# Performance work log

Hardware: AMD Instinct MI355X
Metric: run time of the kernel (lower is better)

## Reference

```python
import jax, jax.numpy as jnp
import numpy as np

N = 100000      # nodes
E = 1_600_000   # edges (avg degree 16)
IN, HID, OUT = 128, 128, 64


def _prep(edge_index, n):
    """Add self-loops and compute symmetric GCN normalization per edge."""
    loops = jnp.arange(n, dtype=edge_index.dtype)
    src = jnp.concatenate([edge_index[0], loops])  # [E+N]
    dst = jnp.concatenate([edge_index[1], loops])  # [E+N]
    deg = jax.ops.segment_sum(jnp.ones(src.shape, jnp.float32), dst, num_segments=n)
    dinv = jnp.where(deg > 0, jax.lax.rsqrt(deg), 0.0)
    norm = dinv[src] * dinv[dst]                   # [E+N]
    return src, dst, norm


def gcn_conv(x, src, dst, norm, W, b, n):
    # PyG GCNConv: transform first, then normalized gather/scatter-add aggregate
    h = x @ W                                      # [N, C_out]
    msg = h[src] * norm[:, None]                   # [E+N, C_out] irregular gather
    return jax.ops.segment_sum(msg, dst, num_segments=n) + b


def setup_inputs() -> dict:
    key = jax.random.key(0)
    k1, k2, k3, k4 = jax.random.split(key, 4)
    x = jax.random.normal(k1, (N, IN), dtype=jnp.float32)
    edge_index = jax.random.randint(k2, (2, E), 0, N, dtype=jnp.int32)
    W1 = jax.random.normal(k3, (IN, HID), dtype=jnp.float32) * (1.0 / np.sqrt(IN))
    b1 = jnp.zeros((HID,), jnp.float32)
    W2 = jax.random.normal(k4, (HID, OUT), dtype=jnp.float32) * (1.0 / np.sqrt(HID))
    b2 = jnp.zeros((OUT,), jnp.float32)
    return {"x": x, "W1": W1, "b1": b1, "W2": W2, "b2": b2, "edge_index": edge_index}


def reference(x, W1, b1, W2, b2, edge_index):
    n = x.shape[0]
    src, dst, norm = _prep(edge_index, n)
    h = gcn_conv(x, src, dst, norm, W1, b1, n)
    h = jax.nn.softmax(h, axis=1)
    return gcn_conv(h, src, dst, norm, W2, b2, n)
```

## Files before the change

### kernel.cpp

```cpp
#include <hip/hip_runtime.h>
#include <hip/hip_fp16.h>
#include <cstdint>
#include <cstddef>


#define BSHIFT 8
#define NBPAD 512
#define NWG 256
#define CAP 6144

typedef _Float16 half8 __attribute__((ext_vector_type(8)));
typedef float f32x4 __attribute__((ext_vector_type(4)));

__device__ __forceinline__ void h8_to_f(const uint4& u, float* f) {
  const __half2* hp = (const __half2*)&u;
#pragma unroll
  for (int i = 0; i < 4; ++i) {
    float2 t = __half22float2(hp[i]);
    f[2 * i] = t.x;
    f[2 * i + 1] = t.y;
  }
}

__device__ __forceinline__ void fma8(float* acc, float w, const float* v) {
#pragma unroll
  for (int i = 0; i < 8; ++i) acc[i] = fmaf(w, v[i], acc[i]);
}

__device__ __forceinline__ int block_scan256(int v, int* wsums) {
  const int lane = threadIdx.x & 63;
  const int wid = threadIdx.x >> 6;
  int x = v;
#pragma unroll
  for (int d = 1; d < 64; d <<= 1) {
    int y = __shfl_up(x, d);
    if (lane >= d) x += y;
  }
  if (lane == 63) wsums[wid] = x;
  __syncthreads();
  int off = 0;
#pragma unroll
  for (int j = 0; j < 4; ++j)
    if (j < wid) off += wsums[j];
  return off + x;
}

__global__ __launch_bounds__(256) void wg_count(const int* __restrict__ dst,
                                                int* __restrict__ counts,
                                                int E, int nb, int slice) {
  __shared__ int lh[NBPAD];
  const int w = blockIdx.x;
  for (int i = threadIdx.x; i < nb; i += 256) lh[i] = 0;
  __syncthreads();
  const int e0 = w * slice;
  const int e1 = min(e0 + slice, E);
  for (int e = e0 + threadIdx.x; e < e1; e += 256)
    atomicAdd(&lh[dst[e] >> BSHIFT], 1);
  __syncthreads();
  for (int i = threadIdx.x; i < nb; i += 256) counts[(size_t)w * NBPAD + i] = lh[i];
}

__global__ __launch_bounds__(256) void cell_scan(const int* __restrict__ counts,
                                                 int* __restrict__ cur,
                                                 int* __restrict__ btotal, int nb) {
  __shared__ int wsums[4];
  const int b = blockIdx.x;
  const int tid = threadIdx.x;
  int v = counts[(size_t)tid * NBPAD + b];
  int incl = block_scan256(v, wsums);
  cur[(size_t)tid * NBPAD + b] = incl - v;
  if (tid == 255) btotal[b] = incl;
}

__global__ __launch_bounds__(1024) void bscan(const int* __restrict__ btotal,
                                              int* __restrict__ bstart,
                                              int* __restrict__ row_start,
                                              int nb, int n, int E) {
  __shared__ int wsum[16];
  const int tid = threadIdx.x;
  const int lane = tid & 63;
  const int wid = tid >> 6;
  int v = (tid < nb) ? btotal[tid] : 0;
  int x = v;
#pragma unroll
  for (int d = 1; d < 64; d <<= 1) {
    int y = __shfl_up(x, d);
    if (lane >= d) x += y;
  }
  if (lane == 63) wsum[wid] = x;
  __syncthreads();
  if (wid == 0) {
    int w = (lane < 16) ? wsum[lane] : 0;
#pragma unroll
    for (int d = 1; d < 16; d <<= 1) {
      int y = __shfl_up(w, d);
      if (lane >= d) w += y;
    }
    if (lane < 16) wsum[lane] = w;
  }
  __syncthreads();
  int boff = (wid > 0) ? wsum[wid - 1] : 0;
  int incl = boff + x;
  if (tid < nb) {
    bstart[tid] = incl - v;
    if (tid == nb - 1) bstart[nb] = incl;
  }
  if (tid == 0) row_start[n] = E;
}

__global__ __launch_bounds__(256) void wg_scatter(const int* __restrict__ src,
                                                  const int* __restrict__ dst,
                                                  const int* __restrict__ cur,
                                                  const int* __restrict__ bstart,
                                                  unsigned* __restrict__ staging,
                                                  int E, int nb, int slice) {
  __shared__ int lc[NBPAD];
  const int w = blockIdx.x;
  for (int i = threadIdx.x; i < nb; i += 256)
    lc[i] = cur[(size_t)w * NBPAD + i] + bstart[i];
  __syncthreads();
  const int e0 = w * slice;
  const int e1 = min(e0 + slice, E);
  for (int e = e0 + threadIdx.x; e < e1; e += 256) {
    int d = dst[e];
    int p = atomicAdd(&lc[d >> BSHIFT], 1);
    staging[p] = ((unsigned)(d & 255) << 24) | (unsigned)src[e];
  }
}

__global__ __launch_bounds__(256) void bucket_hist(const unsigned* __restrict__ staging,
                                                   const int* __restrict__ bstart,
                                                   int* __restrict__ row_start,
                                                   float* __restrict__ dinv, int n) {
  __shared__ int lcnt[256];
  __shared__ int wsums[4];
  const int b = blockIdx.x;
  const int tid = threadIdx.x;
  const int n0 = b << BSHIFT;
  const int s0 = bstart[b];
  const int cnt = bstart[b + 1] - s0;

  lcnt[tid] = 0;
  __syncthreads();
  for (int i = tid; i < cnt; i += 256)
    atomicAdd(&lcnt[staging[s0 + i] >> 24], 1);
  __syncthreads();

  const int v = lcnt[tid];
  const int incl = block_scan256(v, wsums);
  const int node = n0 + tid;
  if (node < n) {
    row_start[node] = s0 + incl - v;
    dinv[node] = rsqrtf((float)v + 1.0f);
  }
}

__global__ __launch_bounds__(256) void bucket_pack(const unsigned* __restrict__ staging,
                                                   const int* __restrict__ bstart,
                                                   const int* __restrict__ row_start,
                                                   const float* __restrict__ dinv,
                                                   int2* __restrict__ pack, int n) {
  __shared__ int lcur[256];
  __shared__ int lbuf[CAP];
  const int b = blockIdx.x;
  const int tid = threadIdx.x;
  const int n0 = b << BSHIFT;
  const int s0 = bstart[b];
  const int cnt = bstart[b + 1] - s0;

  const int node = n0 + tid;
  lcur[tid] = (node < n) ? (row_start[node] - s0) : 0;
  __syncthreads();

  for (int i = tid; i < cnt; i += 256) {
    unsigned p = staging[s0 + i];
    int pos = atomicAdd(&lcur[p >> 24], 1);
    int s = (int)(p & 0xFFFFFFu);
    if (pos < CAP) lbuf[pos] = s;
    else pack[s0 + pos] = make_int2(s, __float_as_int(dinv[s]));
  }
  __syncthreads();
  const int lim = cnt < CAP ? cnt : CAP;
  for (int i = tid; i < lim; i += 256) {
    int s = lbuf[i];
    pack[s0 + i] = make_int2(s, __float_as_int(dinv[s]));
  }
}

template <int M>
__global__ __launch_bounds__(256) void pack_w(const float* __restrict__ W,
                                              _Float16* __restrict__ Wp) {
  int e = blockIdx.x * 256 + threadIdx.x;
  if (e < 128 * M) {
    int k = e / M, c = e % M;
    int t = k >> 5, g = (k >> 3) & 3, j = k & 7;
    Wp[(((size_t)t * M + c) * 4 + g) * 8 + j] = (_Float16)W[e];
  }
}

template <int M, bool HIN>
__global__ __launch_bounds__(256) void gemm_mfma(const void* __restrict__ Xp,
                                                 const _Float16* __restrict__ Wp,
                                                 _Float16* __restrict__ H, int N) {
  constexpr int CT = M / 16;
  const int wave = threadIdx.x >> 6;
  const int lane = threadIdx.x & 63;
  const int row0 = (blockIdx.x * 4 + wave) * 16;
  if (row0 >= N) return;
  const int r = lane & 15;
  const int g = lane >> 4;
  int row = row0 + r;
  if (row >= N) row = N - 1;

  f32x4 acc[CT];
#pragma unroll
  for (int c = 0; c < CT; ++c) acc[c] = (f32x4){0.f, 0.f, 0.f, 0.f};

#pragma unroll
  for (int t = 0; t < 4; ++t) {
    half8 a;
    if constexpr (HIN) {
      a = *(const half8*)((const _Float16*)Xp + (size_t)row * 128 + t * 32 + g * 8);
    } else {
      const float* xp = (const float*)Xp + (size_t)row * 128 + t * 32 + g * 8;
      float4 x0 = *(const float4*)xp;
      float4 x1 = *(const float4*)(xp + 4);
      a[0] = (_Float16)x0.x; a[1] = (_Float16)x0.y;
      a[2] = (_Float16)x0.z; a[3] = (_Float16)x0.w;
      a[4] = (_Float16)x1.x; a[5] = (_Float16)x1.y;
      a[6] = (_Float16)x1.z; a[7] = (_Float16)x1.w;
    }
#pragma unroll
    for (int c = 0; c < CT; ++c) {
      half8 b = *(const half8*)(Wp + (((size_t)t * M + c * 16 + r) * 4 + g) * 8);
      acc[c] = __builtin_amdgcn_mfma_f32_16x16x32_f16(a, b, acc[c], 0, 0, 0);
    }
  }

#pragma unroll
  for (int c = 0; c < CT; ++c) {
#pragma unroll
    for (int i = 0; i < 4; ++i) {
      int rr = row0 + 4 * g + i;
      if (rr < N) H[(size_t)rr * M + c * 16 + r] = (_Float16)acc[c][i];
    }
  }
}

__device__ __forceinline__ void pack_batch(const int2* __restrict__ pack,
                                           int e, int e1, int2* p) {
#pragma unroll
  for (int j = 0; j < 4; ++j) {
    int idx = e + j;
    bool ok = idx < e1;
    p[j] = pack[ok ? idx : (e1 - 1)];
    if (!ok) p[j].y = 0;
  }
}

template <int F, bool SM, bool OUTHALF>
__global__ __launch_bounds__(256) void aggregate(const __half* __restrict__ h,
                                                 const int* __restrict__ row_start,
                                                 const int2* __restrict__ pack,
                                                 const float* __restrict__ dinv,
                                                 const float* __restrict__ bias,
                                                 void* __restrict__ out, int n) {
  constexpr int LPG = F / 8;
  constexpr int GPB = 256 / LPG;
  const int node = blockIdx.x * GPB + (int)(threadIdx.x / LPG);
  const int lane = threadIdx.x % LPG;
  if (node >= n) return;

  const uint4* hv = (const uint4*)h;
  const float di = dinv[node];

  float acc[8];
  {
    uint4 su = hv[(size_t)node * LPG + lane];
    float sf[8];
    h8_to_f(su, sf);
#pragma unroll
    for (int i = 0; i < 8; ++i) acc[i] = di * sf[i];
  }

  const int e0 = row_start[node];
  const int e1 = row_start[node + 1];
  const int nbat = (e1 - e0 + 3) >> 2;

  if (nbat > 0) {
    int2 p0[4], p1[4];
    uint4 r0[4];
    pack_batch(pack, e0, e1, p0);
#pragma unroll
    for (int j = 0; j < 4; ++j) r0[j] = hv[(size_t)p0[j].x * LPG + lane];
    if (nbat > 1) pack_batch(pack, e0 + 4, e1, p1);

    for (int k = 0; k < nbat; ++k) {
      uint4 r1[4];
      if (k + 1 < nbat) {
#pragma unroll
        for (int j = 0; j < 4; ++j) r1[j] = hv[(size_t)p1[j].x * LPG + lane];
      }
      int2 p2[4];
      if (k + 2 < nbat) pack_batch(pack, e0 + 4 * (k + 2), e1, p2);
#pragma unroll
      for (int j = 0; j < 4; ++j) {
        float v[8];
        h8_to_f(r0[j], v);
        fma8(acc, __int_as_float(p0[j].y), v);
      }
#pragma unroll
      for (int j = 0; j < 4; ++j) {
        p0[j] = p1[j];
        p1[j] = p2[j];
        r0[j] = r1[j];
      }
    }
  }

  {
    const float4* bv = (const float4*)bias;
    float4 b0 = bv[lane * 2], b1 = bv[lane * 2 + 1];
    acc[0] = fmaf(di, acc[0], b0.x);
    acc[1] = fmaf(di, acc[1], b0.y);
    acc[2] = fmaf(di, acc[2], b0.z);
    acc[3] = fmaf(di, acc[3], b0.w);
    acc[4] = fmaf(di, acc[4], b1.x);
    acc[5] = fmaf(di, acc[5], b1.y);
    acc[6] = fmaf(di, acc[6], b1.z);
    acc[7] = fmaf(di, acc[7], b1.w);
  }

  if constexpr (SM) {
    float m = acc[0];
#pragma unroll
    for (int i = 1; i < 8; ++i) m = fmaxf(m, acc[i]);
#pragma unroll
    for (int off = LPG / 2; off >= 1; off >>= 1) m = fmaxf(m, __shfl_xor(m, off));
    float ex[8], ssum = 0.f;
#pragma unroll
    for (int i = 0; i < 8; ++i) {
      ex[i] = __expf(acc[i] - m);
      ssum += ex[i];
    }
#pragma unroll
    for (int off = LPG / 2; off >= 1; off >>= 1) ssum += __shfl_xor(ssum, off);
    float r = 1.0f / ssum;
#pragma unroll
    for (int i = 0; i < 8; ++i) acc[i] = ex[i] * r;
  }

  if constexpr (OUTHALF) {
    union { __half2 h2[4]; uint4 u; } cv;
#pragma unroll
    for (int i = 0; i < 4; ++i)
      cv.h2[i] = __floats2half2_rn(acc[2 * i], acc[2 * i + 1]);
    ((uint4*)out)[(size_t)node * LPG + lane] = cv.u;
  } else {
    float4* ov = (float4*)out;
    ov[(size_t)node * (F / 4) + lane * 2] =
        make_float4(acc[0], acc[1], acc[2], acc[3]);
    ov[(size_t)node * (F / 4) + lane * 2 + 1] =
        make_float4(acc[4], acc[5], acc[6], acc[7]);
  }
}

extern "C" void kernel_launch(void* const* d_in, const int* in_sizes, int n_in,
                              void* d_out, int out_size, void* d_ws, size_t ws_size,
                              hipStream_t stream) {
  const float* x  = (const float*)d_in[0];
  const float* W1 = (const float*)d_in[1];
  const float* b1 = (const float*)d_in[2];
  const float* W2 = (const float*)d_in[3];
  const float* b2 = (const float*)d_in[4];
  const int*   ei = (const int*)d_in[5];

  const int N = in_sizes[0] / 128;
  const int E = in_sizes[5] / 2;
  const int NB = (N + 255) >> BSHIFT;
  const int SLICE = (E + NWG - 1) / NWG;
  const int* srcp = ei;
  const int* dstp = ei + E;

  auto align256 = [](size_t v) { return (v + 255) & ~(size_t)255; };
  char* ws = (char*)d_ws;
  size_t o_dinv   = 0;
  size_t o_rs     = align256(o_dinv + (size_t)N * 4);
  size_t o_cnts   = align256(o_rs + (size_t)(N + 1) * 4);
  size_t o_cur    = align256(o_cnts + (size_t)NWG * NBPAD * 4);
  size_t o_btot   = align256(o_cur + (size_t)NWG * NBPAD * 4);
  size_t o_bstart = align256(o_btot + (size_t)NBPAD * 4);
  size_t o_wp1    = align256(o_bstart + (size_t)(NBPAD + 1) * 4);
  size_t o_wp2    = align256(o_wp1 + (size_t)128 * 128 * 2);
  size_t o_stg    = align256(o_wp2 + (size_t)128 * 64 * 2);
  size_t o_pack   = align256(o_stg + (size_t)E * 4);
  size_t o_h1     = align256(o_pack + (size_t)E * 8);
  size_t o_s      = align256(o_h1 + (size_t)N * 128 * 2);

  float*    dinv     = (float*)(ws + o_dinv);
  int*      rowstart = (int*)(ws + o_rs);
  int*      counts   = (int*)(ws + o_cnts);
  int*      cur      = (int*)(ws + o_cur);
  int*      btotal   = (int*)(ws + o_btot);
  int*      bstart   = (int*)(ws + o_bstart);
  _Float16* wp1      = (_Float16*)(ws + o_wp1);
  _Float16* wp2      = (_Float16*)(ws + o_wp2);
  unsigned* staging  = (unsigned*)(ws + o_stg);
  int2*     pack     = (int2*)(ws + o_pack);
  _Float16* h1       = (_Float16*)(ws + o_h1);
  _Float16* sbuf     = (_Float16*)(ws + o_s);

  wg_count<<<NWG, 256, 0, stream>>>(dstp, counts, E, NB, SLICE);
  cell_scan<<<NB, 256, 0, stream>>>(counts, cur, btotal, NB);
  bscan<<<1, 1024, 0, stream>>>(btotal, bstart, rowstart, NB, N, E);
  wg_scatter<<<NWG, 256, 0, stream>>>(srcp, dstp, cur, bstart, staging, E, NB, SLICE);
  bucket_hist<<<NB, 256, 0, stream>>>(staging, bstart, rowstart, dinv, N);
  bucket_pack<<<NB, 256, 0, stream>>>(staging, bstart, rowstart, dinv, pack, N);

  pack_w<128><<<(128 * 128 + 255) / 256, 256, 0, stream>>>(W1, wp1);
  pack_w<64><<<(128 * 64 + 255) / 256, 256, 0, stream>>>(W2, wp2);

  gemm_mfma<128, false><<<(N + 63) / 64, 256, 0, stream>>>(x, wp1, h1, N);
  aggregate<128, true, true><<<(N + 15) / 16, 256, 0, stream>>>(
      (const __half*)h1, rowstart, pack, dinv, b1, sbuf, N);
  gemm_mfma<64, true><<<(N + 63) / 64, 256, 0, stream>>>(sbuf, wp2, h1, N);
  aggregate<64, false, false><<<(N + 31) / 32, 256, 0, stream>>>(
      (const __half*)h1, rowstart, pack, dinv, b2, d_out, N);
}
```

Baseline: 192.4 us.

## Fold source-degree scaling into GEMM epilogue and shrink edge pack to indices

The dinv[src] factor of the symmetric normalization is now applied once per row in the GEMM epilogue, so the aggregation does plain adds instead of per-edge weighted FMAs. The per-edge pack array drops from int2 (index plus weight) to a bare int index, halving index traffic in both aggregation passes and in bucket_pack. Padded tail edges now point at an extra zero row appended to each feature buffer, which is cleared with memsets. This adds a separate h2 buffer and a per-row dinv load in the GEMMs, and multiplying before the fp16 store changes rounding slightly.

Result: no change. 195.8 us (+1.7%).

```diff
diff --git a/kernel.cpp b/kernel.cpp
--- a/kernel.cpp
+++ b/kernel.cpp
@@ -22,9 +22,9 @@
   }
 }
 
-__device__ __forceinline__ void fma8(float* acc, float w, const float* v) {
-#pragma unroll
-  for (int i = 0; i < 8; ++i) acc[i] = fmaf(w, v[i], acc[i]);
+__device__ __forceinline__ void add8(float* acc, const float* v) {
+#pragma unroll
+  for (int i = 0; i < 8; ++i) acc[i] += v[i];
 }
 
 __device__ __forceinline__ int block_scan256(int v, int* wsums) {
@@ -158,8 +158,7 @@
 __global__ __launch_bounds__(256) void bucket_pack(const unsigned* __restrict__ staging,
                                                    const int* __restrict__ bstart,
                                                    const int* __restrict__ row_start,
-                                                   const float* __restrict__ dinv,
-                                                   int2* __restrict__ pack, int n) {
+                                                   int* __restrict__ pack, int n) {
   __shared__ int lcur[256];
   __shared__ int lbuf[CAP];
   const int b = blockIdx.x;
@@ -177,14 +176,11 @@
     int pos = atomicAdd(&lcur[p >> 24], 1);
     int s = (int)(p & 0xFFFFFFu);
     if (pos < CAP) lbuf[pos] = s;
-    else pack[s0 + pos] = make_int2(s, __float_as_int(dinv[s]));
+    else pack[s0 + pos] = s;
   }
   __syncthreads();
   const int lim = cnt < CAP ? cnt : CAP;
-  for (int i = tid; i < lim; i += 256) {
-    int s = lbuf[i];
-    pack[s0 + i] = make_int2(s, __float_as_int(dinv[s]));
-  }
+  for (int i = tid; i < lim; i += 256) pack[s0 + i] = lbuf[i];
 }
 
 template <int M>
@@ -201,6 +197,7 @@
 template <int M, bool HIN>
 __global__ __launch_bounds__(256) void gemm_mfma(const void* __restrict__ Xp,
                                                  const _Float16* __restrict__ Wp,
+                                                 const float* __restrict__ dscale,
                                                  _Float16* __restrict__ H, int N) {
   constexpr int CT = M / 16;
   const int wave = threadIdx.x >> 6;
@@ -237,31 +234,37 @@
     }
   }
 
+  float ds[4];
+#pragma unroll
+  for (int i = 0; i < 4; ++i) {
+    int rr = row0 + 4 * g + i;
+    ds[i] = (rr < N) ? dscale[rr] : 0.f;
+  }
 #pragma unroll
   for (int c = 0; c < CT; ++c) {
 #pragma unroll
     for (int i = 0; i < 4; ++i) {
       int rr = row0 + 4 * g + i;
-      if (rr < N) H[(size_t)rr * M + c * 16 + r] = (_Float16)acc[c][i];
-    }
-  }
-}
-
-__device__ __forceinline__ void pack_batch(const int2* __restrict__ pack,
-                                           int e, int e1, int2* p) {
+      if (rr < N) H[(size_t)rr * M + c * 16 + r] = (_Float16)(acc[c][i] * ds[i]);
+    }
+  }
+}
+
+__device__ __forceinline__ void pack_batch(const int* __restrict__ pack,
+                                           int e, int e1, int zrow, int* p) {
 #pragma unroll
   for (int j = 0; j < 4; ++j) {
     int idx = e + j;
     bool ok = idx < e1;
-    p[j] = pack[ok ? idx : (e1 - 1)];
-    if (!ok) p[j].y = 0;
+    int s = pack[ok ? idx : (e1 - 1)];
+    p[j] = ok ? s : zrow;
   }
 }
 
 template <int F, bool SM, bool OUTHALF>
 __global__ __launch_bounds__(256) void aggregate(const __half* __restrict__ h,
                                                  const int* __restrict__ row_start,
-                                                 const int2* __restrict__ pack,
+                                                 const int* __restrict__ pack,
                                                  const float* __restrict__ dinv,
                                                  const float* __restrict__ bias,
                                                  void* __restrict__ out, int n) {
@@ -273,14 +276,12 @@
 
   const uint4* hv = (const uint4*)h;
   const float di = dinv[node];
+  const int zrow = n;
 
   float acc[8];
   {
     uint4 su = hv[(size_t)node * LPG + lane];
-    float sf[8];
-    h8_to_f(su, sf);
-#pragma unroll
-    for (int i = 0; i < 8; ++i) acc[i] = di * sf[i];
+    h8_to_f(su, acc);
   }
 
   const int e0 = row_start[node];
@@ -288,26 +289,26 @@
   const int nbat = (e1 - e0 + 3) >> 2;
 
   if (nbat > 0) {
-    int2 p0[4], p1[4];
+    int p0[4], p1[4];
     uint4 r0[4];
-    pack_batch(pack, e0, e1, p0);
-#pragma unroll
-    for (int j = 0; j < 4; ++j) r0[j] = hv[(size_t)p0[j].x * LPG + lane];
-    if (nbat > 1) pack_batch(pack, e0 + 4, e1, p1);
+    pack_batch(pack, e0, e1, zrow, p0);
+#pragma unroll
+    for (int j = 0; j < 4; ++j) r0[j] = hv[(size_t)p0[j] * LPG + lane];
+    if (nbat > 1) pack_batch(pack, e0 + 4, e1, zrow, p1);
 
     for (int k = 0; k < nbat; ++k) {
       uint4 r1[4];
       if (k + 1 < nbat) {
 #pragma unroll
-        for (int j = 0; j < 4; ++j) r1[j] = hv[(size_t)p1[j].x * LPG + lane];
+        for (int j = 0; j < 4; ++j) r1[j] = hv[(size_t)p1[j] * LPG + lane];
       }
-      int2 p2[4];
-      if (k + 2 < nbat) pack_batch(pack, e0 + 4 * (k + 2), e1, p2);
+      int p2[4];
+      if (k + 2 < nbat) pack_batch(pack, e0 + 4 * (k + 2), e1, zrow, p2);
 #pragma unroll
       for (int j = 0; j < 4; ++j) {
         float v[8];
         h8_to_f(r0[j], v);
-        fma8(acc, __int_as_float(p0[j].y), v);
+        add8(acc, v);
       }
 #pragma unroll
       for (int j = 0; j < 4; ++j) {
@@ -394,8 +395,9 @@
   size_t o_wp2    = align256(o_wp1 + (size_t)128 * 128 * 2);
   size_t o_stg    = align256(o_wp2 + (size_t)128 * 64 * 2);
   size_t o_pack   = align256(o_stg + (size_t)E * 4);
-  size_t o_h1     = align256(o_pack + (size_t)E * 8);
-  size_t o_s      = align256(o_h1 + (size_t)N * 128 * 2);
+  size_t o_h1     = align256(o_pack + (size_t)E * 4);
+  size_t o_h2     = align256(o_h1 + (size_t)(N + 1) * 128 * 2);
+  size_t o_s      = align256(o_h2 + (size_t)(N + 1) * 64 * 2);
 
   float*    dinv     = (float*)(ws + o_dinv);
   int*      rowstart = (int*)(ws + o_rs);
@@ -406,24 +408,28 @@
   _Float16* wp1      = (_Float16*)(ws + o_wp1);
   _Float16* wp2      = (_Float16*)(ws + o_wp2);
   unsigned* staging  = (unsigned*)(ws + o_stg);
-  int2*     pack     = (int2*)(ws + o_pack);
+  int*      pack     = (int*)(ws + o_pack);
   _Float16* h1       = (_Float16*)(ws + o_h1);
+  _Float16* h2       = (_Float16*)(ws + o_h2);
   _Float16* sbuf     = (_Float16*)(ws + o_s);
+
+  hipMemsetAsync(h1 + (size_t)N * 128, 0, 128 * 2, stream);
+  hipMemsetAsync(h2 + (size_t)N * 64, 0, 64 * 2, stream);
 
   wg_count<<<NWG, 256, 0, stream>>>(dstp, counts, E, NB, SLICE);
   cell_scan<<<NB, 256, 0, stream>>>(counts, cur, btotal, NB);
   bscan<<<1, 1024, 0, stream>>>(btotal, bstart, rowstart, NB, N, E);
   wg_scatter<<<NWG, 256, 0, stream>>>(srcp, dstp, cur, bstart, staging, E, NB, SLICE);
   bucket_hist<<<NB, 256, 0, stream>>>(staging, bstart, rowstart, dinv, N);
-  bucket_pack<<<NB, 256, 0, stream>>>(staging, bstart, rowstart, dinv, pack, N);
+  bucket_pack<<<NB, 256, 0, stream>>>(staging, bstart, rowstart, pack, N);
 
   pack_w<128><<<(128 * 128 + 255) / 256, 256, 0, stream>>>(W1, wp1);
   pack_w<64><<<(128 * 64 + 255) / 256, 256, 0, stream>>>(W2, wp2);
 
-  gemm_mfma<128, false><<<(N + 63) / 64, 256, 0, stream>>>(x, wp1, h1, N);
+  gemm_mfma<128, false><<<(N + 63) / 64, 256, 0, stream>>>(x, wp1, dinv, h1, N);
   aggregate<128, true, true><<<(N + 15) / 16, 256, 0, stream>>>(
       (const __half*)h1, rowstart, pack, dinv, b1, sbuf, N);
-  gemm_mfma<64, true><<<(N + 63) / 64, 256, 0, stream>>>(sbuf, wp2, h1, N);
+  gemm_mfma<64, true><<<(N + 63) / 64, 256, 0, stream>>>(sbuf, wp2, dinv, h2, N);
   aggregate<64, false, false><<<(N + 31) / 32, 256, 0, stream>>>(
-      (const __half*)h1, rowstart, pack, dinv, b2, d_out, N);
-}
+      (const __half*)h2, rowstart, pack, dinv, b2, d_out, N);
+}
```
